# Kernel optimization log

Hardware: AMD Instinct MI355X
Metric: run time of the kernel (lower is better)

Reference implementation:

```python
import jax, jax.numpy as jnp
import numpy as np

INTER = 256
TEMPERATURE = 4.0
NEG_FILL = -1e9


def setup_inputs() -> dict:
    key = jax.random.key(0)
    ks = jax.random.split(key, 8)
    B, C, H, W = 8, 512, 64, 64
    x_query = jax.random.normal(ks[0], (B, C, H, W), dtype=jnp.float32)
    x_support = jax.random.normal(ks[1], (B, C, H, W), dtype=jnp.float32)
    support_embedding = jax.random.normal(ks[2], (B, INTER, H, W), dtype=jnp.float32)
    support_mask = jax.random.randint(ks[3], (B, 1, H, W), 0, 2).astype(jnp.float32)
    scale = 1.0 / np.sqrt(C)
    theta_w = jax.random.normal(ks[4], (INTER, C), dtype=jnp.float32) * scale
    theta_b = jax.random.normal(ks[5], (INTER,), dtype=jnp.float32) * 0.01
    phi_w = jax.random.normal(ks[6], (INTER, C), dtype=jnp.float32) * scale
    phi_b = jax.random.normal(ks[7], (INTER,), dtype=jnp.float32) * 0.01
    return {
        "x_query": x_query,
        "x_support": x_support,
        "support_embedding": support_embedding,
        "support_mask": support_mask,
        "theta_w": theta_w,
        "theta_b": theta_b,
        "phi_w": phi_w,
        "phi_b": phi_b,
    }


def reference(x_query, x_support, support_embedding, support_mask, theta_w, theta_b, phi_w, phi_b):
    B, C, H, W = x_query.shape
    N = H * W
    # g_x: [B, N, 256]
    g_x = support_embedding.reshape(B, INTER, N).transpose(0, 2, 1)
    # 1x1 convs == per-pixel linear over channels
    theta_x = jnp.einsum('oc,bcn->bno', theta_w, x_query.reshape(B, C, N)) + theta_b  # [B, N, 256]
    phi_x = jnp.einsum('oc,bcn->bon', phi_w, x_support.reshape(B, C, N)) + phi_b[None, :, None]  # [B, 256, N]
    f = jnp.matmul(theta_x, phi_x)  # [B, N, N]
    mask = support_mask.reshape(B, 1, N)
    f = f * mask
    # equality-based mask fill (matches torch masked_fill(f == 0, -1e9))
    f = jnp.where(f == 0, NEG_FILL, f) / TEMPERATURE
    attn = jax.nn.softmax(f, axis=-1)  # dropout is identity in eval mode
    y = jnp.matmul(attn, g_x)  # [B, N, 256]
    y = y.transpose(0, 2, 1).reshape(B, INTER, H, W)
    return y
```

## Files before the change

### kernel.cpp

```cpp
#include <hip/hip_runtime.h>
#include <hip/hip_fp16.h>
#include <stdint.h>

typedef _Float16 f16x8 __attribute__((ext_vector_type(8)));
typedef _Float16 f16x4 __attribute__((ext_vector_type(4)));
typedef float    f32x4 __attribute__((ext_vector_type(4)));

#define MFMA16(a, b, c) __builtin_amdgcn_mfma_f32_16x16x32_f16(a, b, c, 0, 0, 0)

static constexpr int BN   = 8;
static constexpr int CIN  = 512;
static constexpr int NHW  = 4096;
static constexpr int OD   = 256;
static constexpr int KBLK = 32;

#define RSWZ(row, cb) ((((row) << 7)) + ((cb) ^ (((row) & 7) << 4)))

__device__ __forceinline__ f16x8 cvt8(const float4 a, const float4 b) {
    f16x8 r;
    r[0] = (_Float16)a.x; r[1] = (_Float16)a.y; r[2] = (_Float16)a.z; r[3] = (_Float16)a.w;
    r[4] = (_Float16)b.x; r[5] = (_Float16)b.y; r[6] = (_Float16)b.z; r[7] = (_Float16)b.w;
    return r;
}

__device__ __forceinline__ uint32_t pkh2(float x, float y) {
    union { _Float16 h[2]; uint32_t u; } z;
    z.h[0] = (_Float16)x; z.h[1] = (_Float16)y;
    return z.u;
}

__global__ __launch_bounds__(256)
void wcvt(const float* __restrict__ thw, const float* __restrict__ phw,
          _Float16* __restrict__ wf)
{
    const int i = blockIdx.x * 256 + threadIdx.x;
    const float4 a = ((const float4*)thw)[i];
    const float4 b = ((const float4*)phw)[i];
    f16x4 ra, rb;
    ra[0] = (_Float16)a.x; ra[1] = (_Float16)a.y; ra[2] = (_Float16)a.z; ra[3] = (_Float16)a.w;
    rb[0] = (_Float16)b.x; rb[1] = (_Float16)b.y; rb[2] = (_Float16)b.z; rb[3] = (_Float16)b.w;
    *(f16x4*)(wf + (size_t)i * 4)          = ra;
    *(f16x4*)(wf + 131072 + (size_t)i * 4) = rb;
}

__global__ __launch_bounds__(256)
void prep_gemm(const float* __restrict__ xq, const float* __restrict__ xs,
               const _Float16* __restrict__ wf,
               const float* __restrict__ thb, const float* __restrict__ phb,
               _Float16* __restrict__ Qws, _Float16* __restrict__ Kws)
{
    const int nt = blockIdx.x, z = blockIdx.y;
    const int b = z >> 1, sel = z & 1;
    const float* x        = (sel ? xs : xq) + (size_t)b * CIN * NHW;
    const _Float16* w     = wf + (size_t)sel * (OD * CIN);
    const float* bias     = sel ? phb : thb;
    _Float16* out         = (sel ? Kws : Qws) + (size_t)b * NHW * OD;
    const int n0 = nt * 64;

    __shared__ __align__(16) char Xs[64 * 128];
    __shared__ __align__(16) char Ws[256 * 128];

    const int t    = threadIdx.x;
    const int lane = t & 63, wave = t >> 6;
    const int l16  = lane & 15, lh = lane >> 4;

    f32x4 acc[4][4] = {};

    for (int c0 = 0; c0 < CIN; c0 += 64) {
        #pragma unroll
        for (int rep = 0; rep < 4; ++rep) {
            const int ci = rep * 16 + (t >> 4);
            const int nl = (t & 15) * 4;
            const float4 v = *(const float4*)&x[(size_t)(c0 + ci) * NHW + n0 + nl];
            *(_Float16*)(Xs + RSWZ(nl + 0, ci * 2)) = (_Float16)v.x;
            *(_Float16*)(Xs + RSWZ(nl + 1, ci * 2)) = (_Float16)v.y;
            *(_Float16*)(Xs + RSWZ(nl + 2, ci * 2)) = (_Float16)v.z;
            *(_Float16*)(Xs + RSWZ(nl + 3, ci * 2)) = (_Float16)v.w;
        }
        #pragma unroll
        for (int r = 0; r < 8; ++r) {
            const int u = r * 256 + t;
            const int o = u >> 3, cs8 = (u & 7) * 8;
            const f16x8 v = *(const f16x8*)(w + (size_t)o * CIN + c0 + cs8);
            *(f16x8*)(Ws + RSWZ(o, cs8 * 2)) = v;
        }
        __syncthreads();

        #pragma unroll
        for (int kk = 0; kk < 2; ++kk) {
            f16x8 af[4];
            #pragma unroll
            for (int oo = 0; oo < 4; ++oo)
                af[oo] = *(const f16x8*)(Ws + RSWZ(wave * 64 + oo * 16 + l16, kk * 64 + lh * 16));
            #pragma unroll
            for (int nn = 0; nn < 4; ++nn) {
                const f16x8 bf = *(const f16x8*)(Xs + RSWZ(nn * 16 + l16, kk * 64 + lh * 16));
                #pragma unroll
                for (int oo = 0; oo < 4; ++oo)
                    acc[oo][nn] = MFMA16(af[oo], bf, acc[oo][nn]);
            }
        }
        __syncthreads();
    }

    #pragma unroll
    for (int oo = 0; oo < 4; ++oo) {
        const float4 bi = *(const float4*)&bias[wave * 64 + oo * 16 + lh * 4];
        #pragma unroll
        for (int nn = 0; nn < 4; ++nn) {
            f16x4 v;
            v[0] = (_Float16)(acc[oo][nn][0] + bi.x);
            v[1] = (_Float16)(acc[oo][nn][1] + bi.y);
            v[2] = (_Float16)(acc[oo][nn][2] + bi.z);
            v[3] = (_Float16)(acc[oo][nn][3] + bi.w);
            const int n = n0 + nn * 16 + l16;
            *(f16x4*)&out[(size_t)n * OD + wave * 64 + oo * 16 + lh * 4] = v;
        }
    }
}

__global__ __launch_bounds__(256)
void compact_mask(const float* __restrict__ mask, int* __restrict__ idx,
                  int* __restrict__ nbArr)
{
    const int b = blockIdx.x, t = threadIdx.x;
    const float* mb = mask + (size_t)b * NHW;
    __shared__ int cnt[256];
    __shared__ int pre[257];

    const int base = t * 16;
    float mv[16];
    int c = 0;
    #pragma unroll
    for (int i = 0; i < 16; ++i) { mv[i] = mb[base + i]; c += (mv[i] != 0.0f); }
    cnt[t] = c;
    __syncthreads();
    if (t == 0) {
        int s = 0;
        for (int i = 0; i < 256; ++i) { pre[i] = s; s += cnt[i]; }
        pre[256] = s;
    }
    __syncthreads();
    int o = pre[t];
    #pragma unroll
    for (int i = 0; i < 16; ++i)
        if (mv[i] != 0.0f) idx[(size_t)b * NHW + o++] = base + i;

    const int Nb = pre[256];
    const int Npad = (Nb + 63) & ~63;
    for (int k = Nb + t; k < Npad; k += 256) idx[(size_t)b * NHW + k] = 0;
    if (t == 0) { nbArr[b * 2] = Nb; nbArr[b * 2 + 1] = Npad >> 5; }
}

__global__ __launch_bounds__(256)
void gather_kv(const _Float16* __restrict__ Kws, const float* __restrict__ emb,
               const int* __restrict__ idx, const int* __restrict__ nbArr,
               _Float16* __restrict__ Kc, _Float16* __restrict__ Vc)
{
    const int b = blockIdx.y, k0 = blockIdx.x * 64, t = threadIdx.x;
    const int Nb = nbArr[b * 2];
    const int Npad = (Nb + 63) & ~63;
    if (k0 >= Npad) return;

    __shared__ int sidx[64];
    if (t < 64) sidx[t] = idx[(size_t)b * NHW + k0 + t];
    __syncthreads();

    const _Float16* Kb = Kws + (size_t)b * NHW * OD;
    char* KcB = (char*)(Kc + (size_t)b * NHW * OD);
    #pragma unroll
    for (int r = 0; r < 8; ++r) {
        const int u = r * 256 + t;
        const int row = u >> 5, c16 = u & 31;
        const f16x8 v = *(const f16x8*)(Kb + (size_t)sidx[row] * OD + c16 * 8);
        *(f16x8*)(KcB + (size_t)(k0 + row) * 512 + ((c16 * 16) ^ ((row & 7) << 4))) = v;
    }

    const float* eb = emb + (size_t)b * OD * NHW;
    char* VcB = (char*)(Vc + (size_t)b * OD * NHW);
    #pragma unroll
    for (int r = 0; r < 8; ++r) {
        const int u = r * 256 + t;
        const int o = u >> 3, uc = u & 7;
        const int chunk = uc >> 2, uin = uc & 3;
        float4 a, c;
        #pragma unroll
        for (int i = 0; i < 4; ++i) ((float*)&a)[i] = eb[(size_t)o * NHW + sidx[uc * 8 + i]];
        #pragma unroll
        for (int i = 0; i < 4; ++i) ((float*)&c)[i] = eb[(size_t)o * NHW + sidx[uc * 8 + 4 + i]];
        const f16x8 v = cvt8(a, c);
        *(f16x8*)(VcB + (size_t)o * (NHW * 2) + (size_t)k0 * 2 + chunk * 64
                      + ((uin ^ ((o >> 1) & 3)) * 16)) = v;
    }
}

__device__ __forceinline__ void stage_dma(const char* __restrict__ Kb,
                                          const char* __restrict__ Vb,
                                          int j, int t, int wbase,
                                          char* Kld, char* Vld)
{
    typedef __attribute__((address_space(1))) const unsigned int gu32;
    typedef __attribute__((address_space(3))) unsigned int lu32;
    const char* kb = Kb + (size_t)j * (KBLK * 512);
    #pragma unroll
    for (int r = 0; r < 2; ++r) {
        __builtin_amdgcn_global_load_lds(
            (gu32*)(kb + (size_t)(r * 512 + t) * 16),
            (lu32*)(Kld + (r * 512 + wbase) * 16), 16, 0, 0);
    }
    #pragma unroll
    for (int r = 0; r < 2; ++r) {
        const int u = r * 512 + t, o = u >> 2, sl = u & 3;
        __builtin_amdgcn_global_load_lds(
            (gu32*)(Vb + (size_t)o * (NHW * 2) + (size_t)j * 64 + sl * 16),
            (lu32*)(Vld + (r * 512 + wbase) * 16), 16, 0, 0);
    }
}

__global__ __launch_bounds__(512, 2)
void flash_attn(const _Float16* __restrict__ Qws, const _Float16* __restrict__ Kc,
                const _Float16* __restrict__ Vc, const int* __restrict__ nbArr,
                _Float16* __restrict__ Op0, _Float16* __restrict__ Op1,
                float* __restrict__ Sarr)
{
    const int bid = blockIdx.x;
    const int b = bid & 7, u = bid >> 3;
    const int qt = u >> 1, half = u & 1;
    const int t = threadIdx.x, lane = t & 63, wave = t >> 6;
    const int l16 = lane & 15, lh = lane >> 4;
    const int wbase = wave << 6;

    __shared__ __align__(16) char Kl[2][KBLK * 512];
    __shared__ __align__(16) char Vl[2][OD * 64];

    const _Float16* Qb = Qws + (size_t)b * NHW * OD;
    const char* Kb = (const char*)(Kc + (size_t)b * NHW * OD);
    const char* Vb = (const char*)(Vc + (size_t)b * OD * NHW);
    const int Nb = nbArr[b * 2];
    const int nt = nbArr[b * 2 + 1];
    const int nth = (nt + 1) >> 1;
    const int j0 = half ? nth : 0;
    const int j1 = half ? nt : nth;
    const int nl = j1 - j0;

    f16x8 qf[8][2];
    #pragma unroll
    for (int g = 0; g < 2; ++g) {
        const _Float16* qrow = Qb
            + (size_t)(qt * 256 + wave * 32 + g * 16 + l16) * OD + lh * 8;
        #pragma unroll
        for (int kk = 0; kk < 8; ++kk) qf[kk][g] = *(const f16x8*)(qrow + kk * 32);
    }

    f32x4 accO[16][2] = {};
    float M0 = -INFINITY, L0 = 0.f;
    float M1 = -INFINITY, L1 = 0.f;

    stage_dma(Kb, Vb, j0, t, wbase, Kl[0], Vl[0]);
    __syncthreads();

    #pragma unroll 1
    for (int i = 0; i < nl; ++i) {
        const int jt = j0 + i;
        const int cur = i & 1;
        if (i + 1 < nl) stage_dma(Kb, Vb, jt + 1, t, wbase, Kl[cur ^ 1], Vl[cur ^ 1]);

        f32x4 S[2][2] = {};
        #pragma unroll
        for (int ct = 0; ct < 2; ++ct) {
            const int row = ct * 16 + l16;
            #pragma unroll
            for (int kk = 0; kk < 8; ++kk) {
                const f16x8 kf = *(const f16x8*)(Kl[cur] + row * 512
                                     + ((kk * 64 + lh * 16) ^ ((row & 7) << 4)));
                S[ct][0] = MFMA16(kf, qf[kk][0], S[ct][0]);
                S[ct][1] = MFMA16(kf, qf[kk][1], S[ct][1]);
            }
        }

        const bool tail = (jt * 32 + 32 > Nb);
        float lg[8][2];
        #pragma unroll
        for (int ct = 0; ct < 2; ++ct)
            #pragma unroll
            for (int r = 0; r < 4; ++r) {
                float v0 = S[ct][0][r] * 0.25f;
                float v1 = S[ct][1][r] * 0.25f;
                if (tail) {
                    const int kg = jt * 32 + ct * 16 + lh * 4 + r;
                    if (kg >= Nb) { v0 = -1e30f; v1 = -1e30f; }
                }
                lg[ct * 4 + r][0] = v0;
                lg[ct * 4 + r][1] = v1;
            }

        float m80 = lg[0][0], m81 = lg[0][1];
        #pragma unroll
        for (int i2 = 1; i2 < 8; ++i2) { m80 = fmaxf(m80, lg[i2][0]); m81 = fmaxf(m81, lg[i2][1]); }
        m80 = fmaxf(m80, __shfl_xor(m80, 16));
        m80 = fmaxf(m80, __shfl_xor(m80, 32));
        m81 = fmaxf(m81, __shfl_xor(m81, 16));
        m81 = fmaxf(m81, __shfl_xor(m81, 32));

        if (__any((m80 > M0 + 8.0f) || (m81 > M1 + 8.0f))) {
            const float nm0 = fmaxf(M0, m80), nm1 = fmaxf(M1, m81);
            const float f0 = __expf(M0 - nm0), f1 = __expf(M1 - nm1);
            M0 = nm0; L0 *= f0; M1 = nm1; L1 *= f1;
            #pragma unroll
            for (int oo = 0; oo < 16; ++oo)
                #pragma unroll
                for (int r = 0; r < 4; ++r) {
                    accO[oo][0][r] *= f0;
                    accO[oo][1][r] *= f1;
                }
        }

        float s0 = 0.f, s1 = 0.f;
        #pragma unroll
        for (int i2 = 0; i2 < 8; ++i2) {
            lg[i2][0] = __expf(lg[i2][0] - M0); s0 += lg[i2][0];
            lg[i2][1] = __expf(lg[i2][1] - M1); s1 += lg[i2][1];
        }
        s0 += __shfl_xor(s0, 16); s0 += __shfl_xor(s0, 32); L0 += s0;
        s1 += __shfl_xor(s1, 16); s1 += __shfl_xor(s1, 32); L1 += s1;

        const int src0 = l16 + (((2 * lh) & 3) << 4);
        const int src1 = src0 + 16;
        const bool hi = (lh & 2) != 0;
        f16x8 pf[2];
        #pragma unroll
        for (int g = 0; g < 2; ++g) {
            const uint32_t ps0 = pkh2(lg[0][g], lg[1][g]), ps1 = pkh2(lg[2][g], lg[3][g]);
            const uint32_t ps2 = pkh2(lg[4][g], lg[5][g]), ps3 = pkh2(lg[6][g], lg[7][g]);
            const uint32_t a0 = __shfl(ps0, src0), a2 = __shfl(ps2, src0);
            const uint32_t a1 = __shfl(ps1, src0), a3 = __shfl(ps3, src0);
            const uint32_t b0 = __shfl(ps0, src1), b2 = __shfl(ps2, src1);
            const uint32_t b1 = __shfl(ps1, src1), b3 = __shfl(ps3, src1);
            union { uint32_t u[4]; f16x8 v; } pu;
            pu.u[0] = hi ? a2 : a0;
            pu.u[1] = hi ? a3 : a1;
            pu.u[2] = hi ? b2 : b0;
            pu.u[3] = hi ? b3 : b1;
            pf[g] = pu.v;
        }

        #pragma unroll
        for (int oo = 0; oo < 16; ++oo) {
            const int o = oo * 16 + l16;
            const f16x8 vf = *(const f16x8*)(Vl[cur] + o * 64
                                 + ((lh * 16) ^ (((o >> 1) & 3) << 4)));
            accO[oo][0] = MFMA16(vf, pf[0], accO[oo][0]);
            accO[oo][1] = MFMA16(vf, pf[1], accO[oo][1]);
        }
        __syncthreads();
    }

    _Float16* Od = half ? Op1 : Op0;
    float*    Sd = Sarr + (size_t)half * (BN * NHW) + (size_t)b * NHW;
    const float rl0 = 1.0f / fmaxf(L0, 1e-30f);
    const float rl1 = 1.0f / fmaxf(L1, 1e-30f);
    const int n0 = qt * 256 + wave * 32 + l16;
    if (lh == 0) {
        Sd[n0]      = (L0 > 0.f) ? (M0 + __logf(L0)) : -1e30f;
        Sd[n0 + 16] = (L1 > 0.f) ? (M1 + __logf(L1)) : -1e30f;
    }
    #pragma unroll
    for (int oo = 0; oo < 16; ++oo) {
        #pragma unroll
        for (int r = 0; r < 4; ++r) {
            const int o = oo * 16 + lh * 4 + r;
            _Float16* row = Od + ((size_t)b * OD + o) * NHW;
            row[n0]      = (_Float16)(accO[oo][0][r] * rl0);
            row[n0 + 16] = (_Float16)(accO[oo][1][r] * rl1);
        }
    }
}

__global__ __launch_bounds__(256)
void combine(const _Float16* __restrict__ Op0, const _Float16* __restrict__ Op1,
             const float* __restrict__ Sarr, float* __restrict__ outp)
{
    const int b = blockIdx.y;
    const int n0 = blockIdx.x * 64;
    const int t = threadIdx.x;
    const int nc = n0 + (t & 7) * 8;
    const int ob = t >> 3;
    const float* S0 = Sarr + (size_t)b * NHW;
    const float* S1 = Sarr + (size_t)BN * NHW + (size_t)b * NHW;

    float a0[8], a1[8];
    #pragma unroll
    for (int i = 0; i < 8; ++i) {
        const float s0 = S0[nc + i], s1 = S1[nc + i];
        const float sm = fmaxf(s0, s1);
        const float w0 = __expf(s0 - sm), w1 = __expf(s1 - sm);
        const float inv = 1.0f / (w0 + w1);
        a0[i] = w0 * inv; a1[i] = w1 * inv;
    }
    for (int o = ob; o < OD; o += 32) {
        const size_t base = ((size_t)b * OD + o) * NHW + nc;
        const f16x8 u = *(const f16x8*)(Op0 + base);
        const f16x8 v = *(const f16x8*)(Op1 + base);
        float4 r0, r1;
        r0.x = a0[0] * (float)u[0] + a1[0] * (float)v[0];
        r0.y = a0[1] * (float)u[1] + a1[1] * (float)v[1];
        r0.z = a0[2] * (float)u[2] + a1[2] * (float)v[2];
        r0.w = a0[3] * (float)u[3] + a1[3] * (float)v[3];
        r1.x = a0[4] * (float)u[4] + a1[4] * (float)v[4];
        r1.y = a0[5] * (float)u[5] + a1[5] * (float)v[5];
        r1.z = a0[6] * (float)u[6] + a1[6] * (float)v[6];
        r1.w = a0[7] * (float)u[7] + a1[7] * (float)v[7];
        *(float4*)&outp[base]     = r0;
        *(float4*)&outp[base + 4] = r1;
    }
}

extern "C" void kernel_launch(void* const* d_in, const int* in_sizes, int n_in,
                              void* d_out, int out_size, void* d_ws, size_t ws_size,
                              hipStream_t stream) {
    const float* xq   = (const float*)d_in[0];
    const float* xs   = (const float*)d_in[1];
    const float* emb  = (const float*)d_in[2];
    const float* mask = (const float*)d_in[3];
    const float* thw  = (const float*)d_in[4];
    const float* thb  = (const float*)d_in[5];
    const float* phw  = (const float*)d_in[6];
    const float* phb  = (const float*)d_in[7];
    float* out = (float*)d_out;

    const size_t szT = (size_t)BN * NHW * OD;
    _Float16* Qws = (_Float16*)d_ws;
    _Float16* Kws = Qws + szT;
    _Float16* Kc  = Kws + szT;
    _Float16* Vc  = Kc + szT;
    _Float16* wf  = Vc + szT;
    int* idxArr   = (int*)(wf + 2 * OD * CIN);
    int* nbArr    = idxArr + (size_t)BN * NHW;
    _Float16* Op1 = (_Float16*)(nbArr + 16);
    float* Sarr   = (float*)(Op1 + szT);

    wcvt<<<dim3(128), 256, 0, stream>>>(thw, phw, wf);
    compact_mask<<<dim3(BN), 256, 0, stream>>>(mask, idxArr, nbArr);
    prep_gemm<<<dim3(64, 16), 256, 0, stream>>>(xq, xs, wf, thb, phb, Qws, Kws);
    gather_kv<<<dim3(64, BN), 256, 0, stream>>>(Kws, emb, idxArr, nbArr, Kc, Vc);
    flash_attn<<<dim3(256), 512, 0, stream>>>(Qws, Kc, Vc, nbArr, Kws , Op1, Sarr);
    combine<<<dim3(64, BN), 256, 0, stream>>>(Kws , Op1, Sarr, out);
}
```

Measured before the change: 200.8 us.

## Scatter K directly into compacted layout in projection GEMM; widen attention KV block

The mask compaction kernel now also emits a per-pixel position map. The phi projection epilogue uses it to write only unmasked rows straight into the compacted, swizzled K buffer, so the intermediate full K tensor and its gather pass are gone. The attention kernel now stages 64 keys per DMA step and processes them as two 32-key halves, which halves the barrier and prefetch count per tile. The price is double the LDS for the K/V buffers, which may lower occupancy, plus scattered 8-byte stores in the GEMM epilogue.

```diff
diff --git a/kernel.cpp b/kernel.cpp
--- a/kernel.cpp
+++ b/kernel.cpp
@@ -12,7 +12,7 @@
 static constexpr int CIN  = 512;
 static constexpr int NHW  = 4096;
 static constexpr int OD   = 256;
-static constexpr int KBLK = 32;
+static constexpr int KBLK = 64;
 
 #define RSWZ(row, cb) ((((row) << 7)) + ((cb) ^ (((row) & 7) << 4)))
 
@@ -44,25 +44,68 @@
 }
 
 __global__ __launch_bounds__(256)
+void compact_mask(const float* __restrict__ mask, int* __restrict__ idx,
+                  int* __restrict__ pos, int* __restrict__ nbArr)
+{
+    const int b = blockIdx.x, t = threadIdx.x;
+    const float* mb = mask + (size_t)b * NHW;
+    __shared__ int cnt[256];
+    __shared__ int pre[257];
+
+    const int base = t * 16;
+    float mv[16];
+    int c = 0;
+    #pragma unroll
+    for (int i = 0; i < 16; ++i) { mv[i] = mb[base + i]; c += (mv[i] != 0.0f); }
+    cnt[t] = c;
+    __syncthreads();
+    if (t == 0) {
+        int s = 0;
+        for (int i = 0; i < 256; ++i) { pre[i] = s; s += cnt[i]; }
+        pre[256] = s;
+    }
+    __syncthreads();
+    int o = pre[t];
+    #pragma unroll
+    for (int i = 0; i < 16; ++i) {
+        if (mv[i] != 0.0f) {
+            idx[(size_t)b * NHW + o] = base + i;
+            pos[(size_t)b * NHW + base + i] = o;
+            ++o;
+        } else {
+            pos[(size_t)b * NHW + base + i] = -1;
+        }
+    }
+
+    const int Nb = pre[256];
+    const int Npad = (Nb + 63) & ~63;
+    for (int k = Nb + t; k < Npad; k += 256) idx[(size_t)b * NHW + k] = 0;
+    if (t == 0) { nbArr[b * 2] = Nb; nbArr[b * 2 + 1] = Npad >> 6; }
+}
+
+__global__ __launch_bounds__(256)
 void prep_gemm(const float* __restrict__ xq, const float* __restrict__ xs,
                const _Float16* __restrict__ wf,
                const float* __restrict__ thb, const float* __restrict__ phb,
-               _Float16* __restrict__ Qws, _Float16* __restrict__ Kws)
+               const int* __restrict__ pos,
+               _Float16* __restrict__ Qws, _Float16* __restrict__ Kc)
 {
     const int nt = blockIdx.x, z = blockIdx.y;
     const int b = z >> 1, sel = z & 1;
     const float* x        = (sel ? xs : xq) + (size_t)b * CIN * NHW;
     const _Float16* w     = wf + (size_t)sel * (OD * CIN);
     const float* bias     = sel ? phb : thb;
-    _Float16* out         = (sel ? Kws : Qws) + (size_t)b * NHW * OD;
     const int n0 = nt * 64;
 
     __shared__ __align__(16) char Xs[64 * 128];
     __shared__ __align__(16) char Ws[256 * 128];
+    __shared__ int Ps[64];
 
     const int t    = threadIdx.x;
     const int lane = t & 63, wave = t >> 6;
     const int l16  = lane & 15, lh = lane >> 4;
+
+    if (sel && t < 64) Ps[t] = pos[(size_t)b * NHW + n0 + t];
 
     f32x4 acc[4][4] = {};
 
@@ -103,59 +146,49 @@
         __syncthreads();
     }
 
-    #pragma unroll
-    for (int oo = 0; oo < 4; ++oo) {
-        const float4 bi = *(const float4*)&bias[wave * 64 + oo * 16 + lh * 4];
-        #pragma unroll
-        for (int nn = 0; nn < 4; ++nn) {
-            f16x4 v;
-            v[0] = (_Float16)(acc[oo][nn][0] + bi.x);
-            v[1] = (_Float16)(acc[oo][nn][1] + bi.y);
-            v[2] = (_Float16)(acc[oo][nn][2] + bi.z);
-            v[3] = (_Float16)(acc[oo][nn][3] + bi.w);
-            const int n = n0 + nn * 16 + l16;
-            *(f16x4*)&out[(size_t)n * OD + wave * 64 + oo * 16 + lh * 4] = v;
+    if (!sel) {
+        _Float16* out = Qws + (size_t)b * NHW * OD;
+        #pragma unroll
+        for (int oo = 0; oo < 4; ++oo) {
+            const float4 bi = *(const float4*)&bias[wave * 64 + oo * 16 + lh * 4];
+            #pragma unroll
+            for (int nn = 0; nn < 4; ++nn) {
+                f16x4 v;
+                v[0] = (_Float16)(acc[oo][nn][0] + bi.x);
+                v[1] = (_Float16)(acc[oo][nn][1] + bi.y);
+                v[2] = (_Float16)(acc[oo][nn][2] + bi.z);
+                v[3] = (_Float16)(acc[oo][nn][3] + bi.w);
+                const int n = n0 + nn * 16 + l16;
+                *(f16x4*)&out[(size_t)n * OD + wave * 64 + oo * 16 + lh * 4] = v;
+            }
+        }
+    } else {
+        char* KcB = (char*)(Kc + (size_t)b * NHW * OD);
+        #pragma unroll
+        for (int oo = 0; oo < 4; ++oo) {
+            const float4 bi = *(const float4*)&bias[wave * 64 + oo * 16 + lh * 4];
+            const int o = wave * 64 + oo * 16 + lh * 4;
+            #pragma unroll
+            for (int nn = 0; nn < 4; ++nn) {
+                const int k = Ps[nn * 16 + l16];
+                if (k >= 0) {
+                    f16x4 v;
+                    v[0] = (_Float16)(acc[oo][nn][0] + bi.x);
+                    v[1] = (_Float16)(acc[oo][nn][1] + bi.y);
+                    v[2] = (_Float16)(acc[oo][nn][2] + bi.z);
+                    v[3] = (_Float16)(acc[oo][nn][3] + bi.w);
+                    *(f16x4*)(KcB + (size_t)k * 512
+                              + (((o >> 3) * 16) ^ ((k & 7) << 4))
+                              + ((o >> 2) & 1) * 8) = v;
+                }
+            }
         }
     }
 }
 
 __global__ __launch_bounds__(256)
-void compact_mask(const float* __restrict__ mask, int* __restrict__ idx,
-                  int* __restrict__ nbArr)
-{
-    const int b = blockIdx.x, t = threadIdx.x;
-    const float* mb = mask + (size_t)b * NHW;
-    __shared__ int cnt[256];
-    __shared__ int pre[257];
-
-    const int base = t * 16;
-    float mv[16];
-    int c = 0;
-    #pragma unroll
-    for (int i = 0; i < 16; ++i) { mv[i] = mb[base + i]; c += (mv[i] != 0.0f); }
-    cnt[t] = c;
-    __syncthreads();
-    if (t == 0) {
-        int s = 0;
-        for (int i = 0; i < 256; ++i) { pre[i] = s; s += cnt[i]; }
-        pre[256] = s;
-    }
-    __syncthreads();
-    int o = pre[t];
-    #pragma unroll
-    for (int i = 0; i < 16; ++i)
-        if (mv[i] != 0.0f) idx[(size_t)b * NHW + o++] = base + i;
-
-    const int Nb = pre[256];
-    const int Npad = (Nb + 63) & ~63;
-    for (int k = Nb + t; k < Npad; k += 256) idx[(size_t)b * NHW + k] = 0;
-    if (t == 0) { nbArr[b * 2] = Nb; nbArr[b * 2 + 1] = Npad >> 5; }
-}
-
-__global__ __launch_bounds__(256)
-void gather_kv(const _Float16* __restrict__ Kws, const float* __restrict__ emb,
-               const int* __restrict__ idx, const int* __restrict__ nbArr,
-               _Float16* __restrict__ Kc, _Float16* __restrict__ Vc)
+void gather_v(const float* __restrict__ emb, const int* __restrict__ idx,
+              const int* __restrict__ nbArr, _Float16* __restrict__ Vc)
 {
     const int b = blockIdx.y, k0 = blockIdx.x * 64, t = threadIdx.x;
     const int Nb = nbArr[b * 2];
@@ -165,16 +198,6 @@
     __shared__ int sidx[64];
     if (t < 64) sidx[t] = idx[(size_t)b * NHW + k0 + t];
     __syncthreads();
-
-    const _Float16* Kb = Kws + (size_t)b * NHW * OD;
-    char* KcB = (char*)(Kc + (size_t)b * NHW * OD);
-    #pragma unroll
-    for (int r = 0; r < 8; ++r) {
-        const int u = r * 256 + t;
-        const int row = u >> 5, c16 = u & 31;
-        const f16x8 v = *(const f16x8*)(Kb + (size_t)sidx[row] * OD + c16 * 8);
-        *(f16x8*)(KcB + (size_t)(k0 + row) * 512 + ((c16 * 16) ^ ((row & 7) << 4))) = v;
-    }
 
     const float* eb = emb + (size_t)b * OD * NHW;
     char* VcB = (char*)(Vc + (size_t)b * OD * NHW);
@@ -203,16 +226,16 @@
     typedef __attribute__((address_space(3))) unsigned int lu32;
     const char* kb = Kb + (size_t)j * (KBLK * 512);
     #pragma unroll
-    for (int r = 0; r < 2; ++r) {
+    for (int r = 0; r < 4; ++r) {
         __builtin_amdgcn_global_load_lds(
             (gu32*)(kb + (size_t)(r * 512 + t) * 16),
             (lu32*)(Kld + (r * 512 + wbase) * 16), 16, 0, 0);
     }
     #pragma unroll
-    for (int r = 0; r < 2; ++r) {
-        const int u = r * 512 + t, o = u >> 2, sl = u & 3;
+    for (int r = 0; r < 4; ++r) {
+        const int u = r * 512 + t, o = u >> 3, sl = u & 7;
         __builtin_amdgcn_global_load_lds(
-            (gu32*)(Vb + (size_t)o * (NHW * 2) + (size_t)j * 64 + sl * 16),
+            (gu32*)(Vb + (size_t)o * (NHW * 2) + (size_t)j * 128 + sl * 16),
             (lu32*)(Vld + (r * 512 + wbase) * 16), 16, 0, 0);
     }
 }
@@ -231,7 +254,7 @@
     const int wbase = wave << 6;
 
     __shared__ __align__(16) char Kl[2][KBLK * 512];
-    __shared__ __align__(16) char Vl[2][OD * 64];
+    __shared__ __align__(16) char Vl[2][OD * 128];
 
     const _Float16* Qb = Qws + (size_t)b * NHW * OD;
     const char* Kb = (const char*)(Kc + (size_t)b * NHW * OD);
@@ -256,8 +279,10 @@
     float M0 = -INFINITY, L0 = 0.f;
     float M1 = -INFINITY, L1 = 0.f;
 
-    stage_dma(Kb, Vb, j0, t, wbase, Kl[0], Vl[0]);
-    __syncthreads();
+    if (nl > 0) {
+        stage_dma(Kb, Vb, j0, t, wbase, Kl[0], Vl[0]);
+        __syncthreads();
+    }
 
     #pragma unroll 1
     for (int i = 0; i < nl; ++i) {
@@ -265,92 +290,96 @@
         const int cur = i & 1;
         if (i + 1 < nl) stage_dma(Kb, Vb, jt + 1, t, wbase, Kl[cur ^ 1], Vl[cur ^ 1]);
 
-        f32x4 S[2][2] = {};
-        #pragma unroll
-        for (int ct = 0; ct < 2; ++ct) {
-            const int row = ct * 16 + l16;
-            #pragma unroll
-            for (int kk = 0; kk < 8; ++kk) {
-                const f16x8 kf = *(const f16x8*)(Kl[cur] + row * 512
-                                     + ((kk * 64 + lh * 16) ^ ((row & 7) << 4)));
-                S[ct][0] = MFMA16(kf, qf[kk][0], S[ct][0]);
-                S[ct][1] = MFMA16(kf, qf[kk][1], S[ct][1]);
-            }
-        }
-
-        const bool tail = (jt * 32 + 32 > Nb);
-        float lg[8][2];
-        #pragma unroll
-        for (int ct = 0; ct < 2; ++ct)
-            #pragma unroll
-            for (int r = 0; r < 4; ++r) {
-                float v0 = S[ct][0][r] * 0.25f;
-                float v1 = S[ct][1][r] * 0.25f;
-                if (tail) {
-                    const int kg = jt * 32 + ct * 16 + lh * 4 + r;
-                    if (kg >= Nb) { v0 = -1e30f; v1 = -1e30f; }
+        #pragma unroll
+        for (int hk = 0; hk < 2; ++hk) {
+            f32x4 S[2][2] = {};
+            #pragma unroll
+            for (int ct = 0; ct < 2; ++ct) {
+                const int row = hk * 32 + ct * 16 + l16;
+                #pragma unroll
+                for (int kk = 0; kk < 8; ++kk) {
+                    const f16x8 kf = *(const f16x8*)(Kl[cur] + row * 512
+                                         + ((kk * 64 + lh * 16) ^ ((row & 7) << 4)));
+                    S[ct][0] = MFMA16(kf, qf[kk][0], S[ct][0]);
+                    S[ct][1] = MFMA16(kf, qf[kk][1], S[ct][1]);
                 }
-                lg[ct * 4 + r][0] = v0;
-                lg[ct * 4 + r][1] = v1;
-            }
-
-        float m80 = lg[0][0], m81 = lg[0][1];
-        #pragma unroll
-        for (int i2 = 1; i2 < 8; ++i2) { m80 = fmaxf(m80, lg[i2][0]); m81 = fmaxf(m81, lg[i2][1]); }
-        m80 = fmaxf(m80, __shfl_xor(m80, 16));
-        m80 = fmaxf(m80, __shfl_xor(m80, 32));
-        m81 = fmaxf(m81, __shfl_xor(m81, 16));
-        m81 = fmaxf(m81, __shfl_xor(m81, 32));
-
-        if (__any((m80 > M0 + 8.0f) || (m81 > M1 + 8.0f))) {
-            const float nm0 = fmaxf(M0, m80), nm1 = fmaxf(M1, m81);
-            const float f0 = __expf(M0 - nm0), f1 = __expf(M1 - nm1);
-            M0 = nm0; L0 *= f0; M1 = nm1; L1 *= f1;
-            #pragma unroll
-            for (int oo = 0; oo < 16; ++oo)
+            }
+
+            const int kbase = jt * 64 + hk * 32;
+            const bool tail = (kbase + 32 > Nb);
+            float lg[8][2];
+            #pragma unroll
+            for (int ct = 0; ct < 2; ++ct)
                 #pragma unroll
                 for (int r = 0; r < 4; ++r) {
-                    accO[oo][0][r] *= f0;
-                    accO[oo][1][r] *= f1;
+                    float v0 = S[ct][0][r] * 0.25f;
+                    float v1 = S[ct][1][r] * 0.25f;
+                    if (tail) {
+                        const int kg = kbase + ct * 16 + lh * 4 + r;
+                        if (kg >= Nb) { v0 = -1e30f; v1 = -1e30f; }
+                    }
+                    lg[ct * 4 + r][0] = v0;
+                    lg[ct * 4 + r][1] = v1;
                 }
-        }
-
-        float s0 = 0.f, s1 = 0.f;
-        #pragma unroll
-        for (int i2 = 0; i2 < 8; ++i2) {
-            lg[i2][0] = __expf(lg[i2][0] - M0); s0 += lg[i2][0];
-            lg[i2][1] = __expf(lg[i2][1] - M1); s1 += lg[i2][1];
-        }
-        s0 += __shfl_xor(s0, 16); s0 += __shfl_xor(s0, 32); L0 += s0;
-        s1 += __shfl_xor(s1, 16); s1 += __shfl_xor(s1, 32); L1 += s1;
-
-        const int src0 = l16 + (((2 * lh) & 3) << 4);
-        const int src1 = src0 + 16;
-        const bool hi = (lh & 2) != 0;
-        f16x8 pf[2];
-        #pragma unroll
-        for (int g = 0; g < 2; ++g) {
-            const uint32_t ps0 = pkh2(lg[0][g], lg[1][g]), ps1 = pkh2(lg[2][g], lg[3][g]);
-            const uint32_t ps2 = pkh2(lg[4][g], lg[5][g]), ps3 = pkh2(lg[6][g], lg[7][g]);
-            const uint32_t a0 = __shfl(ps0, src0), a2 = __shfl(ps2, src0);
-            const uint32_t a1 = __shfl(ps1, src0), a3 = __shfl(ps3, src0);
-            const uint32_t b0 = __shfl(ps0, src1), b2 = __shfl(ps2, src1);
-            const uint32_t b1 = __shfl(ps1, src1), b3 = __shfl(ps3, src1);
-            union { uint32_t u[4]; f16x8 v; } pu;
-            pu.u[0] = hi ? a2 : a0;
-            pu.u[1] = hi ? a3 : a1;
-            pu.u[2] = hi ? b2 : b0;
-            pu.u[3] = hi ? b3 : b1;
-            pf[g] = pu.v;
-        }
-
-        #pragma unroll
-        for (int oo = 0; oo < 16; ++oo) {
-            const int o = oo * 16 + l16;
-            const f16x8 vf = *(const f16x8*)(Vl[cur] + o * 64
-                                 + ((lh * 16) ^ (((o >> 1) & 3) << 4)));
-            accO[oo][0] = MFMA16(vf, pf[0], accO[oo][0]);
-            accO[oo][1] = MFMA16(vf, pf[1], accO[oo][1]);
+
+            float m80 = lg[0][0], m81 = lg[0][1];
+            #pragma unroll
+            for (int i2 = 1; i2 < 8; ++i2) { m80 = fmaxf(m80, lg[i2][0]); m81 = fmaxf(m81, lg[i2][1]); }
+            m80 = fmaxf(m80, __shfl_xor(m80, 16));
+            m80 = fmaxf(m80, __shfl_xor(m80, 32));
+            m81 = fmaxf(m81, __shfl_xor(m81, 16));
+            m81 = fmaxf(m81, __shfl_xor(m81, 32));
+
+            if (__any((m80 > M0 + 8.0f) || (m81 > M1 + 8.0f))) {
+                const float nm0 = fmaxf(M0, m80), nm1 = fmaxf(M1, m81);
+                const float f0 = __expf(M0 - nm0), f1 = __expf(M1 - nm1);
+                M0 = nm0; L0 *= f0; M1 = nm1; L1 *= f1;
+                #pragma unroll
+                for (int oo = 0; oo < 16; ++oo)
+                    #pragma unroll
+                    for (int r = 0; r < 4; ++r) {
+                        accO[oo][0][r] *= f0;
+                        accO[oo][1][r] *= f1;
+                    }
+            }
+
+            float s0 = 0.f, s1 = 0.f;
+            #pragma unroll
+            for (int i2 = 0; i2 < 8; ++i2) {
+                lg[i2][0] = __expf(lg[i2][0] - M0); s0 += lg[i2][0];
+                lg[i2][1] = __expf(lg[i2][1] - M1); s1 += lg[i2][1];
+            }
+            s0 += __shfl_xor(s0, 16); s0 += __shfl_xor(s0, 32); L0 += s0;
+            s1 += __shfl_xor(s1, 16); s1 += __shfl_xor(s1, 32); L1 += s1;
+
+            const int src0 = l16 + (((2 * lh) & 3) << 4);
+            const int src1 = src0 + 16;
+            const bool hi = (lh & 2) != 0;
+            f16x8 pf[2];
+            #pragma unroll
+            for (int g = 0; g < 2; ++g) {
+                const uint32_t ps0 = pkh2(lg[0][g], lg[1][g]), ps1 = pkh2(lg[2][g], lg[3][g]);
+                const uint32_t ps2 = pkh2(lg[4][g], lg[5][g]), ps3 = pkh2(lg[6][g], lg[7][g]);
+                const uint32_t a0 = __shfl(ps0, src0), a2 = __shfl(ps2, src0);
+                const uint32_t a1 = __shfl(ps1, src0), a3 = __shfl(ps3, src0);
+                const uint32_t b0 = __shfl(ps0, src1), b2 = __shfl(ps2, src1);
+                const uint32_t b1 = __shfl(ps1, src1), b3 = __shfl(ps3, src1);
+                union { uint32_t u[4]; f16x8 v; } pu;
+                pu.u[0] = hi ? a2 : a0;
+                pu.u[1] = hi ? a3 : a1;
+                pu.u[2] = hi ? b2 : b0;
+                pu.u[3] = hi ? b3 : b1;
+                pf[g] = pu.v;
+            }
+
+            #pragma unroll
+            for (int oo = 0; oo < 16; ++oo) {
+                const int o = oo * 16 + l16;
+                const f16x8 vf = *(const f16x8*)(Vl[cur] + o * 128 + hk * 64
+                                     + ((lh * 16) ^ (((o >> 1) & 3) << 4)));
+                accO[oo][0] = MFMA16(vf, pf[0], accO[oo][0]);
+                accO[oo][1] = MFMA16(vf, pf[1], accO[oo][1]);
+            }
         }
         __syncthreads();
     }
@@ -430,19 +459,20 @@
 
     const size_t szT = (size_t)BN * NHW * OD;
     _Float16* Qws = (_Float16*)d_ws;
-    _Float16* Kws = Qws + szT;
-    _Float16* Kc  = Kws + szT;
+    _Float16* Op0 = Qws + szT;
+    _Float16* Kc  = Op0 + szT;
     _Float16* Vc  = Kc + szT;
     _Float16* wf  = Vc + szT;
     int* idxArr   = (int*)(wf + 2 * OD * CIN);
     int* nbArr    = idxArr + (size_t)BN * NHW;
-    _Float16* Op1 = (_Float16*)(nbArr + 16);
+    int* posArr   = nbArr + 16;
+    _Float16* Op1 = (_Float16*)(posArr + (size_t)BN * NHW);
     float* Sarr   = (float*)(Op1 + szT);
 
     wcvt<<<dim3(128), 256, 0, stream>>>(thw, phw, wf);
-    compact_mask<<<dim3(BN), 256, 0, stream>>>(mask, idxArr, nbArr);
-    prep_gemm<<<dim3(64, 16), 256, 0, stream>>>(xq, xs, wf, thb, phb, Qws, Kws);
-    gather_kv<<<dim3(64, BN), 256, 0, stream>>>(Kws, emb, idxArr, nbArr, Kc, Vc);
-    flash_attn<<<dim3(256), 512, 0, stream>>>(Qws, Kc, Vc, nbArr, Kws , Op1, Sarr);
-    combine<<<dim3(64, BN), 256, 0, stream>>>(Kws , Op1, Sarr, out);
-}
+    compact_mask<<<dim3(BN), 256, 0, stream>>>(mask, idxArr, posArr, nbArr);
+    prep_gemm<<<dim3(64, 16), 256, 0, stream>>>(xq, xs, wf, thb, phb, posArr, Qws, Kc);
+    gather_v<<<dim3(64, BN), 256, 0, stream>>>(emb, idxArr, nbArr, Vc);
+    flash_attn<<<dim3(256), 512, 0, stream>>>(Qws, Kc, Vc, nbArr, Op0, Op1, Sarr);
+    combine<<<dim3(64, BN), 256, 0, stream>>>(Op0, Op1, Sarr, out);
+}
```

New measurement: 214.5 us. +6.8%, slower.
